# Kernel tuning notes

Hardware: AMD Instinct MI355X
Metric: run time of the kernel (lower is better)

## Reference

```python
import jax, jax.numpy as jnp
import numpy as np

N_NODES = 50000
N_EDGES = 800000
NUM_GRAPHS = 512
D_IN = 64
D_H = 64
BN_EPS = 1e-5


def setup_inputs() -> dict:
    key = jax.random.key(0)
    ks = jax.random.split(key, 12)
    x = jax.random.normal(ks[0], (N_NODES, D_IN), dtype=jnp.float32)
    edge_index = jax.random.randint(ks[1], (2, N_EDGES), 0, N_NODES, dtype=jnp.int64)
    batch = jnp.sort(jax.random.randint(ks[2], (N_NODES,), 0, NUM_GRAPHS, dtype=jnp.int64))
    s1 = 1.0 / np.sqrt(D_IN)
    s2 = 1.0 / np.sqrt(D_H)
    s3 = 1.0 / np.sqrt(2 * D_H)
    W1 = jax.random.uniform(ks[3], (D_IN, D_H), jnp.float32, -s1, s1)
    b1 = jax.random.uniform(ks[4], (D_H,), jnp.float32, -s1, s1)
    gamma = jnp.ones((D_H,), jnp.float32)
    beta = jnp.zeros((D_H,), jnp.float32)
    W2 = jax.random.uniform(ks[5], (D_H, D_H), jnp.float32, -s2, s2)
    b2 = jax.random.uniform(ks[6], (D_H,), jnp.float32, -s2, s2)
    Wl1 = jax.random.uniform(ks[7], (2 * D_H, 2 * D_H), jnp.float32, -s3, s3)
    bl1 = jax.random.uniform(ks[8], (2 * D_H,), jnp.float32, -s3, s3)
    Wl2 = jax.random.uniform(ks[9], (2 * D_H, 1), jnp.float32, -s3, s3)
    bl2 = jax.random.uniform(ks[10], (1,), jnp.float32, -s3, s3)
    return {"x": x, "edge_index": edge_index, "batch": batch,
            "W1": W1, "b1": b1, "gamma": gamma, "beta": beta,
            "W2": W2, "b2": b2, "Wl1": Wl1, "bl1": bl1, "Wl2": Wl2, "bl2": bl2}


def reference(x, edge_index, batch, W1, b1, gamma, beta, W2, b2, Wl1, bl1, Wl2, bl2):
    src, dst = edge_index[0], edge_index[1]
    # GINConv with eps=0: (1+eps)*x_i + sum_{j->i} x_j
    agg = x + jax.ops.segment_sum(x[src], dst, num_segments=N_NODES)
    # MLP: Linear -> BatchNorm1d (training stats, biased var) -> ReLU -> Linear -> ReLU
    h = agg @ W1 + b1
    mean = jnp.mean(h, axis=0)
    var = jnp.var(h, axis=0)
    h = (h - mean) * jax.lax.rsqrt(var + BN_EPS) * gamma + beta
    h = jax.nn.relu(h)
    h = jax.nn.relu(h @ W2 + b2)
    # global add/max pooling per graph
    h_add = jax.ops.segment_sum(h, batch, num_segments=NUM_GRAPHS)
    h_max = jax.ops.segment_max(h, batch, num_segments=NUM_GRAPHS)
    g = jnp.concatenate((h_add, h_max), axis=1)  # [G, 2*D_H]
    g = jax.nn.relu(g @ Wl1 + bl1)
    logits = g @ Wl2 + bl2  # [G, 1]
    return (jax.nn.sigmoid(logits), logits)
```

## Files before the change

kernel.cpp:

```cpp
#include <hip/hip_runtime.h>
#include <hip/hip_bf16.h>

#define N_NODES 50000
#define N_EDGES 800000
#define NUM_GRAPHS 512
#define D 64
#define BN_EPS 1e-5f

#define BUK_SHIFT 7
#define BUK_SIZE 128
#define NBUK ((N_NODES + BUK_SIZE - 1) / BUK_SIZE)
#define CHUNK_A 4096
#define NBLK_A ((N_EDGES + CHUNK_A - 1) / CHUNK_A)
#define GBLK ((N_NODES + 63) / 64)

__global__ __launch_bounds__(256) void k_bhist(const int* __restrict__ ei,
                                               int* __restrict__ bcnt) {
    __shared__ int h[NBUK];
    int t = threadIdx.x;
    for (int j = t; j < NBUK; j += 256) h[j] = 0;
    __syncthreads();
    int e0 = blockIdx.x * CHUNK_A;
#pragma unroll
    for (int i = 0; i < CHUNK_A / 256; i++) {
        int e = e0 + i * 256 + t;
        if (e < N_EDGES) atomicAdd(&h[ei[N_EDGES + e] >> BUK_SHIFT], 1);
    }
    __syncthreads();
    for (int j = t; j < NBUK; j += 256)
        if (h[j]) atomicAdd(&bcnt[j], h[j]);
}

__global__ __launch_bounds__(512) void k_bscan(const int* __restrict__ bcnt,
                                               int* __restrict__ boffs,
                                               int* __restrict__ gcur,
                                               int* __restrict__ offs) {
    __shared__ int sm[512];
    int t = threadIdx.x;
    int v = (t < NBUK) ? bcnt[t] : 0;
    sm[t] = v;
    __syncthreads();
    for (int off = 1; off < 512; off <<= 1) {
        int a = sm[t];
        int u = (t >= off) ? sm[t - off] : 0;
        __syncthreads();
        sm[t] = a + u;
        __syncthreads();
    }
    if (t < NBUK) { int ex = sm[t] - v; boffs[t] = ex; gcur[t] = ex; }
    if (t == 0) { boffs[NBUK] = N_EDGES; offs[N_NODES] = N_EDGES; }
}

__global__ __launch_bounds__(256) void k_binA(const int* __restrict__ ei,
                                              int* __restrict__ gcur,
                                              unsigned* __restrict__ pairs) {
    __shared__ int cnt[NBUK];
    __shared__ int base[NBUK];
    int t = threadIdx.x;
    for (int j = t; j < NBUK; j += 256) cnt[j] = 0;
    __syncthreads();
    int e0 = blockIdx.x * CHUNK_A;
    unsigned pd[CHUNK_A / 256];
    int loc[CHUNK_A / 256];
#pragma unroll
    for (int i = 0; i < CHUNK_A / 256; i++) {
        int e = e0 + i * 256 + t;
        pd[i] = 0xFFFFFFFFu;
        if (e < N_EDGES) {
            unsigned s = (unsigned)ei[e];
            unsigned d = (unsigned)ei[N_EDGES + e];
            pd[i] = (d << 16) | s;
            loc[i] = atomicAdd(&cnt[d >> BUK_SHIFT], 1);
        }
    }
    __syncthreads();
    for (int j = t; j < NBUK; j += 256)
        base[j] = cnt[j] ? atomicAdd(&gcur[j], cnt[j]) : 0;
    __syncthreads();
#pragma unroll
    for (int i = 0; i < CHUNK_A / 256; i++) {
        if (pd[i] != 0xFFFFFFFFu) {
            unsigned d = pd[i] >> 16;
            pairs[base[d >> BUK_SHIFT] + loc[i]] =
                ((d & (BUK_SIZE - 1)) << 16) | (pd[i] & 0xFFFFu);
        }
    }
}

__global__ __launch_bounds__(256) void k_sort(const unsigned* __restrict__ pairs,
                                              const int* __restrict__ boffs,
                                              int* __restrict__ offs,
                                              int* __restrict__ esrc) {
    __shared__ int cnt[BUK_SIZE];
    __shared__ int sm[BUK_SIZE];
    __shared__ int cur[BUK_SIZE];
    int b = blockIdx.x, t = threadIdx.x;
    int n0 = b << BUK_SHIFT;
    int nrows = min(BUK_SIZE, N_NODES - n0);
    int e0 = boffs[b], e1 = boffs[b + 1];
    int m = e1 - e0;
    if (t < BUK_SIZE) cnt[t] = 0;
    __syncthreads();
    for (int j = t; j < m; j += 256)
        atomicAdd(&cnt[pairs[e0 + j] >> 16], 1);
    __syncthreads();
    if (t < BUK_SIZE) sm[t] = cnt[t];
    __syncthreads();
    for (int off = 1; off < BUK_SIZE; off <<= 1) {
        int v = 0, u = 0;
        if (t < BUK_SIZE) { v = sm[t]; u = (t >= off) ? sm[t - off] : 0; }
        __syncthreads();
        if (t < BUK_SIZE) sm[t] = v + u;
        __syncthreads();
    }
    if (t < BUK_SIZE) {
        int ex = sm[t] - cnt[t];
        cur[t] = ex;
        if (t < nrows) offs[n0 + t] = e0 + ex;
    }
    __syncthreads();
    for (int j = t; j < m; j += 256) {
        unsigned p = pairs[e0 + j];
        int pos = atomicAdd(&cur[p >> 16], 1);
        esrc[e0 + pos] = (int)(p & 0xFFFFu);
    }
}

__global__ __launch_bounds__(256) void k_gather(const float* __restrict__ x,
                                                const int* __restrict__ offs,
                                                const int* __restrict__ esrc,
                                                float* __restrict__ agg) {
    int wid = (blockIdx.x * 256 + threadIdx.x) >> 6;
    int lane = threadIdx.x & 63;
    if (wid >= N_NODES) return;
    int grp = lane >> 4;
    int f4  = lane & 15;
    const float4* x4 = (const float4*)x;
    int base = offs[wid], end = offs[wid + 1];
    float4 acc = make_float4(0.f, 0.f, 0.f, 0.f);
    int i = base;
    for (; i + 7 < end; i += 8) {
        int s0 = esrc[i + grp];
        int s1 = esrc[i + 4 + grp];
        float4 v0 = x4[(size_t)s0 * 16 + f4];
        float4 v1 = x4[(size_t)s1 * 16 + f4];
        acc.x += v0.x; acc.y += v0.y; acc.z += v0.z; acc.w += v0.w;
        acc.x += v1.x; acc.y += v1.y; acc.z += v1.z; acc.w += v1.w;
    }
    for (; i + 3 < end; i += 4) {
        int s = esrc[i + grp];
        float4 v = x4[(size_t)s * 16 + f4];
        acc.x += v.x; acc.y += v.y; acc.z += v.z; acc.w += v.w;
    }
    int rem = end - i;
    if (grp < rem) {
        int s = esrc[i + grp];
        float4 v = x4[(size_t)s * 16 + f4];
        acc.x += v.x; acc.y += v.y; acc.z += v.z; acc.w += v.w;
    }
    acc.x += __shfl_xor(acc.x, 16, 64); acc.y += __shfl_xor(acc.y, 16, 64);
    acc.z += __shfl_xor(acc.z, 16, 64); acc.w += __shfl_xor(acc.w, 16, 64);
    acc.x += __shfl_xor(acc.x, 32, 64); acc.y += __shfl_xor(acc.y, 32, 64);
    acc.z += __shfl_xor(acc.z, 32, 64); acc.w += __shfl_xor(acc.w, 32, 64);
    if (grp == 0) {
        float4 xn = x4[(size_t)wid * 16 + f4];
        acc.x += xn.x; acc.y += xn.y; acc.z += xn.z; acc.w += xn.w;
        ((float4*)agg)[(size_t)wid * 16 + f4] = acc;
    }
}

__global__ __launch_bounds__(256) void k_gemm1(const float* __restrict__ agg,
                                               const float* __restrict__ W1,
                                               const float* __restrict__ b1,
                                               float* __restrict__ h,
                                               float* __restrict__ partial) {
    __shared__ float xs[64][65];
    __shared__ float shS[4][64], shQ[4][64];
    int blk = blockIdx.x, t = threadIdx.x;
    int r0 = blk * 64;
    const float4* a4 = (const float4*)(agg + (size_t)r0 * D);
    for (int i = t; i < 1024; i += 256) {
        float4 v = a4[i];
        int row = i >> 4, q = (i & 15) * 4;
        xs[row][q] = v.x; xs[row][q + 1] = v.y;
        xs[row][q + 2] = v.z; xs[row][q + 3] = v.w;
    }
    __syncthreads();
    int lane = t & 63, chunk = t >> 6;
    int r = r0 + lane, c0 = chunk * 16;
    float acc[16];
#pragma unroll
    for (int j = 0; j < 16; j++) acc[j] = b1[c0 + j];
#pragma unroll 4
    for (int k = 0; k < D; k++) {
        float v = xs[lane][k];
#pragma unroll
        for (int j = 0; j < 16; j++)
            acc[j] += v * W1[k * D + c0 + j];
    }
    if (r < N_NODES) {
        float* hp = h + (size_t)r * D + c0;
#pragma unroll
        for (int j4 = 0; j4 < 4; j4++) {
            float4 o;
            o.x = acc[j4 * 4]; o.y = acc[j4 * 4 + 1];
            o.z = acc[j4 * 4 + 2]; o.w = acc[j4 * 4 + 3];
            *(float4*)(hp + j4 * 4) = o;
        }
    }
    __syncthreads();
#pragma unroll
    for (int j = 0; j < 16; j++) xs[lane][c0 + j] = acc[j];
    __syncthreads();
    int nval = min(64, N_NODES - r0);
    {
        float s = 0.f, q = 0.f;
        for (int rr = chunk; rr < nval; rr += 4) {
            float v = xs[rr][lane];
            s += v; q += v * v;
        }
        shS[chunk][lane] = s; shQ[chunk][lane] = q;
    }
    __syncthreads();
    if (chunk == 0) {
        float ts = shS[0][lane] + shS[1][lane] + shS[2][lane] + shS[3][lane];
        float tq = shQ[0][lane] + shQ[1][lane] + shQ[2][lane] + shQ[3][lane];
        partial[blk * 128 + lane] = ts;
        partial[blk * 128 + 64 + lane] = tq;
    }
}

__global__ __launch_bounds__(256) void k_bnred(const float* __restrict__ partial,
                                               float* __restrict__ colsum) {
    __shared__ float sm[256];
    int c = blockIdx.x, t = threadIdx.x;
    float s = 0.f;
    for (int b = t; b < GBLK; b += 256) s += partial[b * 128 + c];
    sm[t] = s;
    __syncthreads();
    for (int off = 128; off; off >>= 1) {
        if (t < off) sm[t] += sm[t + off];
        __syncthreads();
    }
    if (t == 0) colsum[c] = sm[0];
}

__global__ __launch_bounds__(64) void k_bnfin(const float* __restrict__ colsum,
                                              const float* __restrict__ gamma,
                                              const float* __restrict__ beta,
                                              float* __restrict__ bnscale,
                                              float* __restrict__ bnshift) {
    int t = threadIdx.x;
    float mean = colsum[t] * (1.0f / N_NODES);
    float var  = colsum[64 + t] * (1.0f / N_NODES) - mean * mean;
    float rstd = rsqrtf(var + BN_EPS);
    float sc = gamma[t] * rstd;
    bnscale[t] = sc;
    bnshift[t] = beta[t] - mean * sc;
}

__device__ __forceinline__ int lower_bound(const int* __restrict__ b, int v) {
    int lo = 0, hi = N_NODES;
    while (lo < hi) {
        int m = (lo + hi) >> 1;
        if (b[m] < v) lo = m + 1; else hi = m;
    }
    return lo;
}

__global__ __launch_bounds__(256) void k_gemm2pool(const float* __restrict__ h,
                                                   const int* __restrict__ batch,
                                                   const float* __restrict__ bnscale,
                                                   const float* __restrict__ bnshift,
                                                   const float* __restrict__ W2,
                                                   const float* __restrict__ b2,
                                                   float* __restrict__ g) {
    __shared__ float xs[64][65];
    __shared__ float bs[64], bb[64];
    __shared__ float shS[4][64], shM[4][64];
    int blk = blockIdx.x, t = threadIdx.x;
    if (t < 64) { bs[t] = bnscale[t]; bb[t] = bnshift[t]; }
    __syncthreads();
    int r0 = blk * 64;
    const float4* a4 = (const float4*)(h + (size_t)r0 * D);
    for (int i = t; i < 1024; i += 256) {
        float4 v = a4[i];
        int row = i >> 4, q = (i & 15) * 4;
        xs[row][q]     = fmaxf(v.x * bs[q]     + bb[q],     0.0f);
        xs[row][q + 1] = fmaxf(v.y * bs[q + 1] + bb[q + 1], 0.0f);
        xs[row][q + 2] = fmaxf(v.z * bs[q + 2] + bb[q + 2], 0.0f);
        xs[row][q + 3] = fmaxf(v.w * bs[q + 3] + bb[q + 3], 0.0f);
    }
    __syncthreads();
    int lane = t & 63, chunk = t >> 6, c0 = chunk * 16;
    float acc[16];
#pragma unroll
    for (int j = 0; j < 16; j++) acc[j] = b2[c0 + j];
#pragma unroll 4
    for (int k = 0; k < D; k++) {
        float v = xs[lane][k];
#pragma unroll
        for (int j = 0; j < 16; j++)
            acc[j] += v * W2[k * D + c0 + j];
    }
#pragma unroll
    for (int j = 0; j < 16; j++) acc[j] = fmaxf(acc[j], 0.0f);
    __syncthreads();
#pragma unroll
    for (int j = 0; j < 16; j++) xs[lane][c0 + j] = acc[j];
    __syncthreads();
    int nval = min(64, N_NODES - r0);
    int gi0 = batch[r0];
    int gi1 = batch[r0 + nval - 1];
    for (int gi = gi0; gi <= gi1; gi++) {
        int a = max(lower_bound(batch, gi) - r0, 0);
        int b = min(lower_bound(batch, gi + 1) - r0, nval);
        float s = 0.f, m = 0.f;
        for (int rr = a + chunk; rr < b; rr += 4) {
            float v = xs[rr][lane];
            s += v; m = fmaxf(m, v);
        }
        shS[chunk][lane] = s; shM[chunk][lane] = m;
        __syncthreads();
        if (chunk == 0 && b > a) {
            float ts = shS[0][lane] + shS[1][lane] + shS[2][lane] + shS[3][lane];
            float tm = fmaxf(fmaxf(shM[0][lane], shM[1][lane]),
                             fmaxf(shM[2][lane], shM[3][lane]));
            atomicAdd(&g[gi * 128 + lane], ts);
            atomicMax((int*)&g[gi * 128 + 64 + lane], __float_as_int(tm));
        }
        __syncthreads();
    }
}

__global__ __launch_bounds__(128) void k_head(const float* __restrict__ g,
                                              const float* __restrict__ Wl1,
                                              const float* __restrict__ bl1,
                                              const float* __restrict__ Wl2,
                                              const float* __restrict__ bl2,
                                              float* __restrict__ out) {
    __shared__ float gv[128];
    __shared__ float red[2];
    int gi = blockIdx.x;
    int t = threadIdx.x;
    gv[t] = g[gi * 128 + t];
    __syncthreads();
    float acc = bl1[t];
#pragma unroll
    for (int k = 0; k < 128; k++)
        acc += gv[k] * Wl1[k * 128 + t];
    acc = fmaxf(acc, 0.0f);
    float part = acc * Wl2[t];
    for (int off = 32; off; off >>= 1) part += __shfl_down(part, off);
    if ((t & 63) == 0) red[t >> 6] = part;
    __syncthreads();
    if (t == 0) {
        float logit = red[0] + red[1] + bl2[0];
        out[gi] = 1.0f / (1.0f + expf(-logit));
        out[NUM_GRAPHS + gi] = logit;
    }
}

extern "C" void kernel_launch(void* const* d_in, const int* in_sizes, int n_in,
                              void* d_out, int out_size, void* d_ws, size_t ws_size,
                              hipStream_t stream) {
    const float* x     = (const float*)d_in[0];
    const int*   ei    = (const int*)d_in[1];
    const int*   batch = (const int*)d_in[2];
    const float* W1    = (const float*)d_in[3];
    const float* b1    = (const float*)d_in[4];
    const float* gamma = (const float*)d_in[5];
    const float* beta  = (const float*)d_in[6];
    const float* W2    = (const float*)d_in[7];
    const float* b2    = (const float*)d_in[8];
    const float* Wl1   = (const float*)d_in[9];
    const float* bl1   = (const float*)d_in[10];
    const float* Wl2   = (const float*)d_in[11];
    const float* bl2   = (const float*)d_in[12];
    float* out = (float*)d_out;

    float* ws = (float*)d_ws;
    float* agg    = ws;
    float* h      = agg + (size_t)N_NODES * D;
    float* gbuf   = h + (size_t)N_NODES * D;
    float* bnscale= gbuf + NUM_GRAPHS * 128;
    float* bnshift= bnscale + 64;
    float* colsum = bnshift + 64;
    int*   bcnt   = (int*)(colsum + 128);
    int*   boffs  = bcnt + NBUK;
    int*   gcur   = boffs + NBUK + 1;
    int*   offs   = gcur + NBUK;
    int*   esrc   = offs + N_NODES + 1;
    float* partial= (float*)(esrc + N_EDGES);
    unsigned* pairs = (unsigned*)h;

    hipMemsetAsync(bcnt, 0, NBUK * sizeof(int), stream);
    hipMemsetAsync(gbuf, 0, NUM_GRAPHS * 128 * sizeof(float), stream);
    k_bhist    <<<NBLK_A, 256, 0, stream>>>(ei, bcnt);
    k_bscan    <<<1, 512, 0, stream>>>(bcnt, boffs, gcur, offs);
    k_binA     <<<NBLK_A, 256, 0, stream>>>(ei, gcur, pairs);
    k_sort     <<<NBUK, 256, 0, stream>>>(pairs, boffs, offs, esrc);
    k_gather   <<<(N_NODES * 64 + 255) / 256, 256, 0, stream>>>(x, offs, esrc, agg);
    k_gemm1    <<<GBLK, 256, 0, stream>>>(agg, W1, b1, h, partial);
    k_bnred    <<<128, 256, 0, stream>>>(partial, colsum);
    k_bnfin    <<<1, 64, 0, stream>>>(colsum, gamma, beta, bnscale, bnshift);
    k_gemm2pool<<<GBLK, 256, 0, stream>>>(h, batch, bnscale, bnshift, W2, b2, gbuf);
    k_head     <<<NUM_GRAPHS, 128, 0, stream>>>(gbuf, Wl1, bl1, Wl2, bl2, out);
}
```

Before: 240.4 us.

## Remap dense GEMM threads to output columns with weights held in registers

In both dense layers each thread now owns one output column and 16 rows. Its 64-element weight column is cached in registers and the activation rows are read from shared memory as float4 broadcasts; before, each thread repeatedly loaded 16 weights per k from global/L1. Column statistics and pooling are reduced straight from registers, which removes the write-back of the result tile to shared memory and its extra barriers. This raises register pressure (64 weights plus 16 accumulators) and so may lower occupancy. The global stores of h change from float4 per thread to scalar stores per row, which are still coalesced across the wave.

```diff
diff --git a/kernel.cpp b/kernel.cpp
--- a/kernel.cpp
+++ b/kernel.cpp
@@ -174,55 +174,59 @@
                                                const float* __restrict__ b1,
                                                float* __restrict__ h,
                                                float* __restrict__ partial) {
-    __shared__ float xs[64][65];
+    __shared__ float xs[64][68];
     __shared__ float shS[4][64], shQ[4][64];
     int blk = blockIdx.x, t = threadIdx.x;
+    int lane = t & 63, w = t >> 6;
     int r0 = blk * 64;
     const float4* a4 = (const float4*)(agg + (size_t)r0 * D);
     for (int i = t; i < 1024; i += 256) {
         float4 v = a4[i];
         int row = i >> 4, q = (i & 15) * 4;
-        xs[row][q] = v.x; xs[row][q + 1] = v.y;
-        xs[row][q + 2] = v.z; xs[row][q + 3] = v.w;
-    }
-    __syncthreads();
-    int lane = t & 63, chunk = t >> 6;
-    int r = r0 + lane, c0 = chunk * 16;
+        *(float4*)&xs[row][q] = v;
+    }
+    float wreg[64];
+#pragma unroll 8
+    for (int k = 0; k < 64; k++) wreg[k] = W1[k * D + lane];
+    float bias = b1[lane];
+    __syncthreads();
+    int wr0 = w * 16;
     float acc[16];
 #pragma unroll
-    for (int j = 0; j < 16; j++) acc[j] = b1[c0 + j];
-#pragma unroll 4
-    for (int k = 0; k < D; k++) {
-        float v = xs[lane][k];
-#pragma unroll
-        for (int j = 0; j < 16; j++)
-            acc[j] += v * W1[k * D + c0 + j];
-    }
-    if (r < N_NODES) {
-        float* hp = h + (size_t)r * D + c0;
-#pragma unroll
-        for (int j4 = 0; j4 < 4; j4++) {
-            float4 o;
-            o.x = acc[j4 * 4]; o.y = acc[j4 * 4 + 1];
-            o.z = acc[j4 * 4 + 2]; o.w = acc[j4 * 4 + 3];
-            *(float4*)(hp + j4 * 4) = o;
-        }
-    }
-    __syncthreads();
-#pragma unroll
-    for (int j = 0; j < 16; j++) xs[lane][c0 + j] = acc[j];
-    __syncthreads();
+    for (int rb = 0; rb < 4; rb++) {
+        float a0 = bias, a1 = bias, a2 = bias, a3 = bias;
+#pragma unroll
+        for (int k4 = 0; k4 < 16; k4++) {
+            const int kk = k4 * 4;
+            float4 x0 = *(const float4*)&xs[wr0 + rb * 4 + 0][kk];
+            float4 x1 = *(const float4*)&xs[wr0 + rb * 4 + 1][kk];
+            float4 x2 = *(const float4*)&xs[wr0 + rb * 4 + 2][kk];
+            float4 x3 = *(const float4*)&xs[wr0 + rb * 4 + 3][kk];
+            float w0 = wreg[kk], w1 = wreg[kk + 1], w2 = wreg[kk + 2], w3 = wreg[kk + 3];
+            a0 += x0.x * w0 + x0.y * w1 + x0.z * w2 + x0.w * w3;
+            a1 += x1.x * w0 + x1.y * w1 + x1.z * w2 + x1.w * w3;
+            a2 += x2.x * w0 + x2.y * w1 + x2.z * w2 + x2.w * w3;
+            a3 += x3.x * w0 + x3.y * w1 + x3.z * w2 + x3.w * w3;
+        }
+        acc[rb * 4 + 0] = a0; acc[rb * 4 + 1] = a1;
+        acc[rb * 4 + 2] = a2; acc[rb * 4 + 3] = a3;
+    }
     int nval = min(64, N_NODES - r0);
-    {
-        float s = 0.f, q = 0.f;
-        for (int rr = chunk; rr < nval; rr += 4) {
-            float v = xs[rr][lane];
-            s += v; q += v * v;
-        }
-        shS[chunk][lane] = s; shQ[chunk][lane] = q;
-    }
-    __syncthreads();
-    if (chunk == 0) {
+#pragma unroll
+    for (int r = 0; r < 16; r++) {
+        int row = r0 + wr0 + r;
+        if (row < N_NODES) h[(size_t)row * D + lane] = acc[r];
+    }
+    float s = 0.f, q = 0.f;
+#pragma unroll
+    for (int r = 0; r < 16; r++) {
+        bool in = (wr0 + r) < nval;
+        float v = in ? acc[r] : 0.f;
+        s += v; q += v * v;
+    }
+    shS[w][lane] = s; shQ[w][lane] = q;
+    __syncthreads();
+    if (w == 0) {
         float ts = shS[0][lane] + shS[1][lane] + shS[2][lane] + shS[3][lane];
         float tq = shQ[0][lane] + shQ[1][lane] + shQ[2][lane] + shQ[3][lane];
         partial[blk * 128 + lane] = ts;
@@ -275,10 +279,11 @@
                                                    const float* __restrict__ W2,
                                                    const float* __restrict__ b2,
                                                    float* __restrict__ g) {
-    __shared__ float xs[64][65];
+    __shared__ float xs[64][68];
     __shared__ float bs[64], bb[64];
     __shared__ float shS[4][64], shM[4][64];
     int blk = blockIdx.x, t = threadIdx.x;
+    int lane = t & 63, w = t >> 6;
     if (t < 64) { bs[t] = bnscale[t]; bb[t] = bnshift[t]; }
     __syncthreads();
     int r0 = blk * 64;
@@ -286,29 +291,38 @@
     for (int i = t; i < 1024; i += 256) {
         float4 v = a4[i];
         int row = i >> 4, q = (i & 15) * 4;
-        xs[row][q]     = fmaxf(v.x * bs[q]     + bb[q],     0.0f);
-        xs[row][q + 1] = fmaxf(v.y * bs[q + 1] + bb[q + 1], 0.0f);
-        xs[row][q + 2] = fmaxf(v.z * bs[q + 2] + bb[q + 2], 0.0f);
-        xs[row][q + 3] = fmaxf(v.w * bs[q + 3] + bb[q + 3], 0.0f);
-    }
-    __syncthreads();
-    int lane = t & 63, chunk = t >> 6, c0 = chunk * 16;
+        v.x = fmaxf(v.x * bs[q]     + bb[q],     0.0f);
+        v.y = fmaxf(v.y * bs[q + 1] + bb[q + 1], 0.0f);
+        v.z = fmaxf(v.z * bs[q + 2] + bb[q + 2], 0.0f);
+        v.w = fmaxf(v.w * bs[q + 3] + bb[q + 3], 0.0f);
+        *(float4*)&xs[row][q] = v;
+    }
+    float wreg[64];
+#pragma unroll 8
+    for (int k = 0; k < 64; k++) wreg[k] = W2[k * D + lane];
+    float bias = b2[lane];
+    __syncthreads();
+    int wr0 = w * 16;
     float acc[16];
 #pragma unroll
-    for (int j = 0; j < 16; j++) acc[j] = b2[c0 + j];
-#pragma unroll 4
-    for (int k = 0; k < D; k++) {
-        float v = xs[lane][k];
-#pragma unroll
-        for (int j = 0; j < 16; j++)
-            acc[j] += v * W2[k * D + c0 + j];
-    }
-#pragma unroll
-    for (int j = 0; j < 16; j++) acc[j] = fmaxf(acc[j], 0.0f);
-    __syncthreads();
-#pragma unroll
-    for (int j = 0; j < 16; j++) xs[lane][c0 + j] = acc[j];
-    __syncthreads();
+    for (int rb = 0; rb < 4; rb++) {
+        float a0 = bias, a1 = bias, a2 = bias, a3 = bias;
+#pragma unroll
+        for (int k4 = 0; k4 < 16; k4++) {
+            const int kk = k4 * 4;
+            float4 x0 = *(const float4*)&xs[wr0 + rb * 4 + 0][kk];
+            float4 x1 = *(const float4*)&xs[wr0 + rb * 4 + 1][kk];
+            float4 x2 = *(const float4*)&xs[wr0 + rb * 4 + 2][kk];
+            float4 x3 = *(const float4*)&xs[wr0 + rb * 4 + 3][kk];
+            float w0 = wreg[kk], w1 = wreg[kk + 1], w2 = wreg[kk + 2], w3 = wreg[kk + 3];
+            a0 += x0.x * w0 + x0.y * w1 + x0.z * w2 + x0.w * w3;
+            a1 += x1.x * w0 + x1.y * w1 + x1.z * w2 + x1.w * w3;
+            a2 += x2.x * w0 + x2.y * w1 + x2.z * w2 + x2.w * w3;
+            a3 += x3.x * w0 + x3.y * w1 + x3.z * w2 + x3.w * w3;
+        }
+        acc[rb * 4 + 0] = fmaxf(a0, 0.0f); acc[rb * 4 + 1] = fmaxf(a1, 0.0f);
+        acc[rb * 4 + 2] = fmaxf(a2, 0.0f); acc[rb * 4 + 3] = fmaxf(a3, 0.0f);
+    }
     int nval = min(64, N_NODES - r0);
     int gi0 = batch[r0];
     int gi1 = batch[r0 + nval - 1];
@@ -316,13 +330,16 @@
         int a = max(lower_bound(batch, gi) - r0, 0);
         int b = min(lower_bound(batch, gi + 1) - r0, nval);
         float s = 0.f, m = 0.f;
-        for (int rr = a + chunk; rr < b; rr += 4) {
-            float v = xs[rr][lane];
+#pragma unroll
+        for (int r = 0; r < 16; r++) {
+            int row = wr0 + r;
+            bool in = (row >= a) && (row < b);
+            float v = in ? acc[r] : 0.f;
             s += v; m = fmaxf(m, v);
         }
-        shS[chunk][lane] = s; shM[chunk][lane] = m;
-        __syncthreads();
-        if (chunk == 0 && b > a) {
+        shS[w][lane] = s; shM[w][lane] = m;
+        __syncthreads();
+        if (w == 0 && b > a) {
             float ts = shS[0][lane] + shS[1][lane] + shS[2][lane] + shS[3][lane];
             float tm = fmaxf(fmaxf(shM[0][lane], shM[1][lane]),
                              fmaxf(shM[2][lane], shM[3][lane]));
```

After: 438.0 us. 82.2% more time.
